# Kernel optimization log

Hardware: AMD Instinct MI355X
Metric: run time of the kernel (lower is better)

## Reference

```python
import jax, jax.numpy as jnp
import numpy as np

DIM = 1024
NUM_HEADS = 16
HEAD_DIM = DIM // NUM_HEADS  # 64
NB_FEATURES = 256


def setup_inputs() -> dict:
    key = jax.random.key(0)
    k1, k2, k3, k4, k5 = jax.random.split(key, 5)
    x = jax.random.normal(k1, (4, 4096, DIM), dtype=jnp.float32)
    # Dense(dim*3, use_bias=False): weight [dim, 3*dim]
    w_qkv = jax.random.normal(k2, (DIM, 3 * DIM), dtype=jnp.float32) / np.sqrt(DIM)
    # Dense(dim) with bias: weight [dim, dim], bias [dim]
    w_out = jax.random.normal(k3, (DIM, DIM), dtype=jnp.float32) / np.sqrt(DIM)
    b_out = jnp.zeros((DIM,), dtype=jnp.float32)
    # random_normal_initializer default stddev=0.05
    proj = 0.05 * jax.random.normal(k4, (NUM_HEADS, HEAD_DIM, NB_FEATURES), dtype=jnp.float32)
    return {"x": x, "w_qkv": w_qkv, "w_out": w_out, "b_out": b_out, "proj": proj}


def _kernel_feature_map(x, proj):
    # x: [B,H,T,D], proj: [H,D,F] -> [B,H,T,F]
    z = jnp.einsum('bhtd,hdf->bhtf', x, proj)
    return jnp.exp(z - jnp.max(z, axis=-1, keepdims=True))


def reference(x, w_qkv, w_out, b_out, proj):
    B, T, _ = x.shape
    qkv = x @ w_qkv  # [B,T,3*DIM]
    q, k, v = jnp.split(qkv, 3, axis=-1)
    # [B,T,H,D] -> [B,H,T,D]
    def to_heads(t):
        return t.reshape(B, T, NUM_HEADS, HEAD_DIM).transpose(0, 2, 1, 3)
    q, k, v = to_heads(q), to_heads(k), to_heads(v)
    q_prime = _kernel_feature_map(q, proj)  # [B,H,T,F]
    k_prime = _kernel_feature_map(k, proj)  # [B,H,T,F]
    kv = jnp.einsum('bhtf,bhtd->bhfd', k_prime, v)  # [B,H,F,D]
    k_sum = jnp.sum(k_prime, axis=2)  # [B,H,F]
    z = 1.0 / (jnp.einsum('bhtf,bhf->bht', q_prime, k_sum) + 1e-6)
    out = jnp.einsum('bhtf,bhfd,bht->bhtd', q_prime, kv, z)
    out = out.transpose(0, 2, 1, 3).reshape(B, T, DIM)
    return out @ w_out + b_out
```

## Files before the change

### kernel.cpp

```cpp
#include <hip/hip_runtime.h>

#define TOK   16384
#define DIM_  1024
#define QKV_N 3072
#define NH    16
#define HD    64
#define NF    256
#define TSEQ  4096
#define NCHUNK 8
#define CH_T  512
#define KVS   68

typedef __attribute__((ext_vector_type(8))) short  bfrag8;
typedef __attribute__((ext_vector_type(4))) float  ffrag4;
typedef __attribute__((ext_vector_type(8))) unsigned short u16x8;
typedef __attribute__((ext_vector_type(4))) unsigned short u16x4;

__device__ __forceinline__ float bf2f(unsigned short u) {
  union { unsigned int i; float f; } c; c.i = ((unsigned int)u) << 16; return c.f;
}
__device__ __forceinline__ unsigned short f2bf(float f) {
  union { float f; unsigned int i; } c; c.f = f;
  unsigned int r = c.i + 0x7FFFu + ((c.i >> 16) & 1u);
  return (unsigned short)(r >> 16);
}

__device__ __forceinline__ void gload16(const unsigned short* g, unsigned short* l) {
  __builtin_amdgcn_global_load_lds(
      (const __attribute__((address_space(1))) unsigned int*)g,
      (__attribute__((address_space(3))) unsigned int*)l, 16, 0, 0);
}

__global__ __launch_bounds__(256)
void transpose_cast(const float* __restrict__ in, unsigned short* __restrict__ out,
                    int R, int C) {
  __shared__ float tile[32][33];
  const size_t batch_off = (size_t)blockIdx.z * R * C;
  const float* bin = in + batch_off;
  unsigned short* bout = out + batch_off;
  const int bc = blockIdx.x * 32, br = blockIdx.y * 32;
  const int tx = threadIdx.x & 31, ty = threadIdx.x >> 5;
  #pragma unroll
  for (int i = 0; i < 32; i += 8)
    tile[ty + i][tx] = bin[(size_t)(br + ty + i) * C + bc + tx];
  __syncthreads();
  #pragma unroll
  for (int i = 0; i < 32; i += 8)
    bout[(size_t)(bc + ty + i) * R + br + tx] = f2bf(tile[tx][ty + i]);
}

__global__ __launch_bounds__(256)
void split_cast(const float* __restrict__ x, unsigned short* __restrict__ a2) {
  const size_t idx = ((size_t)blockIdx.x * 256 + threadIdx.x) * 8;
  const size_t r = idx >> 10;
  const int c = (int)(idx & 1023);
  const float4 v0 = *(const float4*)&x[idx];
  const float4 v1 = *(const float4*)&x[idx + 4];
  const float f[8] = {v0.x, v0.y, v0.z, v0.w, v1.x, v1.y, v1.z, v1.w};
  u16x8 hi, lo;
  #pragma unroll
  for (int e = 0; e < 8; e++) {
    union { float f; unsigned u; } cc; cc.f = f[e];
    const unsigned short h = (unsigned short)(cc.u >> 16);
    union { unsigned u; float f; } hb; hb.u = ((unsigned)h) << 16;
    hi[e] = h; lo[e] = f2bf(f[e] - hb.f);
  }
  *(u16x8*)&a2[r * 2048 + c] = hi;
  *(u16x8*)&a2[r * 2048 + 1024 + c] = lo;
}

#define GPHASE(Q, STG, VMW)                                                        \
  {                                                                                \
    const int ab = arow + (Q) * 2048;                                              \
    bfrag8 a00 = *(const bfrag8*)&lds[b][0][ab + cA0];                             \
    bfrag8 a01 = *(const bfrag8*)&lds[b][0][ab + cA1];                             \
    bfrag8 a10 = *(const bfrag8*)&lds[b][0][ab + 1024 + cA0];                      \
    bfrag8 a11 = *(const bfrag8*)&lds[b][0][ab + 1024 + cA1];                      \
    if ((Q) == 0) {                                                                \
      _Pragma("unroll")                                                            \
      for (int j = 0; j < 4; j++) {                                                \
        bfr[j][0] = *(const bfrag8*)&lds[b][1][brow + j * 1024 + cA0];             \
        bfr[j][1] = *(const bfrag8*)&lds[b][1][brow + j * 1024 + cA1];             \
      }                                                                            \
    }                                                                              \
    STG;                                                                           \
    __builtin_amdgcn_s_barrier();                                                  \
    __builtin_amdgcn_s_setprio(1);                                                 \
    _Pragma("unroll")                                                              \
    for (int j = 0; j < 4; j++) {                                                  \
      acc[(Q)*2][j]   = __builtin_amdgcn_mfma_f32_16x16x32_bf16(a00, bfr[j][0], acc[(Q)*2][j], 0, 0, 0);   \
      acc[(Q)*2][j]   = __builtin_amdgcn_mfma_f32_16x16x32_bf16(a01, bfr[j][1], acc[(Q)*2][j], 0, 0, 0);   \
      acc[(Q)*2+1][j] = __builtin_amdgcn_mfma_f32_16x16x32_bf16(a10, bfr[j][0], acc[(Q)*2+1][j], 0, 0, 0); \
      acc[(Q)*2+1][j] = __builtin_amdgcn_mfma_f32_16x16x32_bf16(a11, bfr[j][1], acc[(Q)*2+1][j], 0, 0, 0); \
    }                                                                              \
    __builtin_amdgcn_s_setprio(0);                                                 \
    asm volatile("s_waitcnt lgkmcnt(0)" ::: "memory");                             \
    VMW;                                                                           \
    __builtin_amdgcn_s_barrier();                                                  \
  }

template<bool BIAS, typename OutT>
__global__ __launch_bounds__(512, 2)
void gemm256(const unsigned short* __restrict__ A,
             const unsigned short* __restrict__ BT,
             const float* __restrict__ bias, OutT* __restrict__ C,
             int M, int N, int K, int KB) {
  __shared__ alignas(16) unsigned short lds[2][2][256 * 64];
  const int tid = threadIdx.x;
  const int w = tid >> 6, lane = tid & 63;
  const int wm = w >> 2, wn = w & 3;
  const int lq = lane >> 4, lr = lane & 15;

  const int nbx = N >> 8;
  const int cpx = (int)gridDim.x >> 3;
  const int bid = (int)blockIdx.x;
  const int swz = (bid & 7) * cpx + (bid >> 3);
  const int m0 = (swz / nbx) << 8;
  const int n0 = (swz % nbx) << 8;
  const int nkt = K >> 6;
  const int mskB = (KB >> 6) - 1;

  const int sr = tid >> 3;
  const int sc = ((tid & 7) ^ (sr & 7)) << 3;
  const unsigned short* gA = A + (size_t)(m0 + sr) * K + sc;
  const unsigned short* gB = BT + (size_t)(n0 + sr) * KB + sc;

  const int swl = (lr & 7) << 3;
  const int cA0 = (lq * 8) ^ swl;
  const int cA1 = (32 + lq * 8) ^ swl;
  const int arow = (wm * 128 + lr) * 64;
  const int brow = (wn * 64 + lr) * 64;

  ffrag4 acc[8][4] = {};
  bfrag8 bfr[4][2];

  auto stage = [&](int bb, int mat, int h, int kt) {
    const int kk = mat ? (kt & mskB) : kt;
    const int str = mat ? KB : K;
    const unsigned short* g = (mat ? gB : gA) + (size_t)(h * 128) * str + (size_t)kk * 64;
    unsigned short* l = &lds[bb][mat][h * 8192 + tid * 8];
    gload16(g, l);
    gload16(g + (size_t)64 * str, l + 4096);
  };

  stage(0, 0, 0, 0); stage(0, 0, 1, 0);
  stage(0, 1, 0, 0); stage(0, 1, 1, 0);
  stage(1, 1, 0, 1); stage(1, 1, 1, 1);
  asm volatile("s_waitcnt vmcnt(4)" ::: "memory");
  __builtin_amdgcn_s_barrier();

  for (int t = 0; t < nkt; ++t) {
    const int b = t & 1;
    const int bn = b ^ 1;
    GPHASE(0, { if (t + 1 < nkt) stage(bn, 0, 0, t + 1); }, {})
    GPHASE(1, { if (t + 1 < nkt) stage(bn, 0, 1, t + 1); }, {})
    GPHASE(2, { if (t + 2 < nkt) stage(b, 1, 0, t + 2); }, {})
    GPHASE(3, { if (t + 2 < nkt) stage(b, 1, 1, t + 2); },
           { if (t < nkt - 2) { asm volatile("s_waitcnt vmcnt(4)" ::: "memory"); }
             else             { asm volatile("s_waitcnt vmcnt(0)" ::: "memory"); } })
  }

  #pragma unroll
  for (int i = 0; i < 8; i++) {
    const int row = m0 + wm * 128 + i * 16 + lq * 4;
    #pragma unroll
    for (int j = 0; j < 4; j++) {
      const int col = n0 + wn * 64 + j * 16 + lr;
      const float bb = BIAS ? bias[col] : 0.f;
      #pragma unroll
      for (int r = 0; r < 4; r++) {
        const float val = acc[i][j][r] + bb;
        if constexpr (sizeof(OutT) == 2) C[(size_t)(row + r) * N + col] = (OutT)f2bf(val);
        else                             C[(size_t)(row + r) * N + col] = (OutT)val;
      }
    }
  }
}

__global__ __launch_bounds__(256, 2)
void kv_mfma_kernel(const unsigned short* __restrict__ qkv,
                    const unsigned short* __restrict__ projT,
                    float* __restrict__ partial) {
  const int c = blockIdx.x, bh = blockIdx.y;
  const int b = bh >> 4, h = bh & 15;
  const int tid = threadIdx.x;
  const int w = tid >> 6, lane = tid & 63;
  const int lq = lane >> 4, lr = lane & 15;
  __shared__ unsigned short kp[256 * 72];
  __shared__ unsigned short vT[80 * 72];
  __shared__ float wmax[64][4];

  const unsigned short* pTg = projT + (size_t)h * (NF * HD);
  bfrag8 bfgP[2][4];
  #pragma unroll
  for (int kc = 0; kc < 2; kc++)
    #pragma unroll
    for (int j = 0; j < 4; j++)
      bfgP[kc][j] = *(const bfrag8*)&pTg[(size_t)(w * 64 + j * 16 + lr) * 64 + kc * 32 + lq * 8];

  for (int idx = tid; idx < 16 * 72; idx += 256) {
    const int r = idx / 72, cc = idx % 72;
    vT[(64 + r) * 72 + cc] = (r == 0 && cc < 64) ? (unsigned short)0x3F80 : (unsigned short)0;
  }
  __syncthreads();

  ffrag4 acc2[4][5];
  #pragma unroll
  for (int i = 0; i < 4; i++)
    #pragma unroll
    for (int j = 0; j < 5; j++) acc2[i][j] = (ffrag4){0.f, 0.f, 0.f, 0.f};

  const size_t rowbase = (size_t)b * TSEQ + (size_t)c * CH_T;

  for (int tt = 0; tt < CH_T / 64; tt++) {
    const int t0 = tt * 64;
    #pragma unroll
    for (int e = 0; e < 2; e++) {
      const int job = e * 256 + tid;
      const int t = job >> 3, d0 = (job & 7) * 8;
      const u16x8 v = *(const u16x8*)&qkv[(rowbase + t0 + t) * QKV_N + 2048 + h * 64 + d0];
      #pragma unroll
      for (int q = 0; q < 8; q++) vT[(d0 + q) * 72 + t] = v[q];
    }
    ffrag4 accZ[4][4];
    #pragma unroll
    for (int i = 0; i < 4; i++)
      #pragma unroll
      for (int j = 0; j < 4; j++) accZ[i][j] = (ffrag4){0.f, 0.f, 0.f, 0.f};
    #pragma unroll
    for (int kc = 0; kc < 2; kc++) {
      bfrag8 af[4];
      #pragma unroll
      for (int i = 0; i < 4; i++)
        af[i] = *(const bfrag8*)&qkv[(rowbase + t0 + i * 16 + lr) * QKV_N + 1024 + h * 64 + kc * 32 + lq * 8];
      #pragma unroll
      for (int i = 0; i < 4; i++)
        #pragma unroll
        for (int j = 0; j < 4; j++)
          accZ[i][j] = __builtin_amdgcn_mfma_f32_16x16x32_bf16(af[i], bfgP[kc][j], accZ[i][j], 0, 0, 0);
    }
    float pmx[4][4];
    #pragma unroll
    for (int i = 0; i < 4; i++)
      #pragma unroll
      for (int r = 0; r < 4; r++) {
        float m = accZ[i][0][r];
        m = fmaxf(m, accZ[i][1][r]); m = fmaxf(m, accZ[i][2][r]); m = fmaxf(m, accZ[i][3][r]);
        pmx[i][r] = m;
      }
    #pragma unroll
    for (int off = 1; off < 16; off <<= 1)
      #pragma unroll
      for (int i = 0; i < 4; i++)
        #pragma unroll
        for (int r = 0; r < 4; r++)
          pmx[i][r] = fmaxf(pmx[i][r], __shfl_xor(pmx[i][r], off, 64));
    if (lr == 0)
      #pragma unroll
      for (int i = 0; i < 4; i++)
        #pragma unroll
        for (int r = 0; r < 4; r++) wmax[i * 16 + lq * 4 + r][w] = pmx[i][r];
    __syncthreads();
    #pragma unroll
    for (int i = 0; i < 4; i++) {
      float rmarr[4];
      #pragma unroll
      for (int r = 0; r < 4; r++) {
        const float4 wv = *(const float4*)&wmax[i * 16 + lq * 4 + r];
        rmarr[r] = fmaxf(fmaxf(wv.x, wv.y), fmaxf(wv.z, wv.w));
      }
      #pragma unroll
      for (int j = 0; j < 4; j++) {
        u16x4 pk;
        #pragma unroll
        for (int r = 0; r < 4; r++) pk[r] = f2bf(__expf(accZ[i][j][r] - rmarr[r]));
        *(u16x4*)&kp[(w * 64 + j * 16 + lr) * 72 + i * 16 + lq * 4] = pk;
      }
    }
    __syncthreads();
    #pragma unroll
    for (int kc = 0; kc < 2; kc++) {
      bfrag8 af2[4], bf2[5];
      #pragma unroll
      for (int i = 0; i < 4; i++)
        af2[i] = *(const bfrag8*)&kp[(w * 64 + i * 16 + lr) * 72 + kc * 32 + lq * 8];
      #pragma unroll
      for (int j = 0; j < 5; j++)
        bf2[j] = *(const bfrag8*)&vT[(j * 16 + lr) * 72 + kc * 32 + lq * 8];
      #pragma unroll
      for (int i = 0; i < 4; i++)
        #pragma unroll
        for (int j = 0; j < 5; j++)
          acc2[i][j] = __builtin_amdgcn_mfma_f32_16x16x32_bf16(af2[i], bf2[j], acc2[i][j], 0, 0, 0);
    }
    __syncthreads();
  }
  float* pbase = partial + (size_t)(bh * NCHUNK + c) * NF * KVS;
  #pragma unroll
  for (int i = 0; i < 4; i++)
    #pragma unroll
    for (int j = 0; j < 5; j++) {
      if (j == 4 && lr != 0) continue;
      const int col = j * 16 + lr;
      #pragma unroll
      for (int r = 0; r < 4; r++)
        pbase[(size_t)(w * 64 + i * 16 + lq * 4 + r) * KVS + col] = acc2[i][j][r];
    }
}

__global__ __launch_bounds__(256)
void kv_reduce_kernel(const float* __restrict__ partial, float* __restrict__ kv) {
  const size_t i = (size_t)blockIdx.x * 256 + threadIdx.x;
  const size_t per_bh = (size_t)NF * KVS;
  const size_t bh = i / per_bh;
  const size_t j = i % per_bh;
  const float* p = partial + bh * NCHUNK * per_bh + j;
  float s = 0.f;
  #pragma unroll
  for (int c = 0; c < NCHUNK; c++) s += p[c * per_bh];
  kv[i] = s;
}

__global__ __launch_bounds__(256, 2)
void q_attn_mfma_kernel(const unsigned short* __restrict__ qkv,
                        const unsigned short* __restrict__ projT,
                        const float* __restrict__ kv,
                        unsigned short* __restrict__ attn) {
  const int c = blockIdx.x, bh = blockIdx.y;
  const int b = bh >> 4, h = bh & 15;
  const int tid = threadIdx.x;
  const int w = tid >> 6, lane = tid & 63;
  const int lq = lane >> 4, lr = lane & 15;
  __shared__ unsigned short qp[64 * 264];
  __shared__ unsigned short kvT[80 * 264];

  {
    const float* kvrow = kv + ((size_t)bh * NF + tid) * KVS;
    #pragma unroll
    for (int d0 = 0; d0 < 64; d0 += 4) {
      const float4 v = *(const float4*)&kvrow[d0];
      kvT[(d0 + 0) * 264 + tid] = f2bf(v.x);
      kvT[(d0 + 1) * 264 + tid] = f2bf(v.y);
      kvT[(d0 + 2) * 264 + tid] = f2bf(v.z);
      kvT[(d0 + 3) * 264 + tid] = f2bf(v.w);
    }
    kvT[64 * 264 + tid] = f2bf(kvrow[64]);
    for (int idx = tid; idx < 15 * 264; idx += 256)
      kvT[65 * 264 + idx] = 0;
  }
  const unsigned short* pTg = projT + (size_t)h * (NF * HD);
  bfrag8 bfg[2][4];
  #pragma unroll
  for (int kc = 0; kc < 2; kc++)
    #pragma unroll
    for (int j = 0; j < 4; j++)
      bfg[kc][j] = *(const bfrag8*)&pTg[(size_t)(w * 64 + j * 16 + lr) * 64 + kc * 32 + lq * 8];
  __syncthreads();

  for (int tt = 0; tt < CH_T / 64; tt++) {
    const size_t rowbase = (size_t)b * TSEQ + (size_t)c * CH_T + (size_t)tt * 64;
    ffrag4 accZ[4][4];
    #pragma unroll
    for (int i = 0; i < 4; i++)
      #pragma unroll
      for (int j = 0; j < 4; j++) accZ[i][j] = (ffrag4){0.f, 0.f, 0.f, 0.f};
    #pragma unroll
    for (int kc = 0; kc < 2; kc++) {
      bfrag8 af[4];
      #pragma unroll
      for (int i = 0; i < 4; i++)
        af[i] = *(const bfrag8*)&qkv[(rowbase + i * 16 + lr) * QKV_N + 0 + h * 64 + kc * 32 + lq * 8];
      #pragma unroll
      for (int i = 0; i < 4; i++)
        #pragma unroll
        for (int j = 0; j < 4; j++)
          accZ[i][j] = __builtin_amdgcn_mfma_f32_16x16x32_bf16(af[i], bfg[kc][j], accZ[i][j], 0, 0, 0);
    }
    #pragma unroll
    for (int i = 0; i < 4; i++)
      #pragma unroll
      for (int j = 0; j < 4; j++)
        #pragma unroll
        for (int r = 0; r < 4; r++)
          qp[(i * 16 + lq * 4 + r) * 264 + w * 64 + j * 16 + lr] = f2bf(__expf(accZ[i][j][r]));
    __syncthreads();
    ffrag4 acc3[5];
    #pragma unroll
    for (int j = 0; j < 5; j++) acc3[j] = (ffrag4){0.f, 0.f, 0.f, 0.f};
    #pragma unroll
    for (int kc = 0; kc < 8; kc++) {
      const bfrag8 afq = *(const bfrag8*)&qp[(w * 16 + lr) * 264 + kc * 32 + lq * 8];
      #pragma unroll
      for (int j = 0; j < 5; j++) {
        const bfrag8 bf3 = *(const bfrag8*)&kvT[(j * 16 + lr) * 264 + kc * 32 + lq * 8];
        acc3[j] = __builtin_amdgcn_mfma_f32_16x16x32_bf16(afq, bf3, acc3[j], 0, 0, 0);
      }
    }
    #pragma unroll
    for (int r = 0; r < 4; r++) {
      const float den = __shfl(acc3[4][r], lane & 48, 64);
      const float z = 1.f / (den + 1e-6f);
      const int t = c * CH_T + tt * 64 + w * 16 + lq * 4 + r;
      unsigned short* orow = attn + ((size_t)b * TSEQ + t) * DIM_ + h * 64;
      #pragma unroll
      for (int j = 0; j < 4; j++)
        orow[j * 16 + lr] = f2bf(acc3[j][r] * z);
    }
    __syncthreads();
  }
}

extern "C" void kernel_launch(void* const* d_in, const int* in_sizes, int n_in,
                              void* d_out, int out_size, void* d_ws, size_t ws_size,
                              hipStream_t stream) {
  const float* x     = (const float*)d_in[0];
  const float* w_qkv = (const float*)d_in[1];
  const float* w_out = (const float*)d_in[2];
  const float* b_out = (const float*)d_in[3];
  const float* proj  = (const float*)d_in[4];
  float* out = (float*)d_out;

  char* ws = (char*)d_ws;
  unsigned short* qkv    = (unsigned short*)ws;
  float*          partial= (float*)(ws + 100663296);
  unsigned short* attn   = (unsigned short*)(ws + 100663296);
  unsigned short* woutT  = (unsigned short*)(ws + 134217728);
  float*          kvbuf  = (float*)(ws + 136314880);

  const bool full = ws_size >= 174587904ULL;
  unsigned short* a2    = (unsigned short*)(ws + 100663296);
  unsigned short* wqkvT = (unsigned short*)(ws + (full ? 167772160 : 134217728));
  unsigned short* projT = (unsigned short*)(ws + (full ? 174063616 : 140771328));

  transpose_cast<<<dim3(QKV_N/32, DIM_/32, 1), 256, 0, stream>>>(w_qkv, wqkvT, DIM_, QKV_N);
  transpose_cast<<<dim3(NF/32, HD/32, NH), 256, 0, stream>>>(proj, projT, HD, NF);

  if (full) {
    split_cast<<<8192, 256, 0, stream>>>(x, a2);
    gemm256<false, unsigned short><<<768, 512, 0, stream>>>(
        a2, wqkvT, nullptr, qkv, TOK, QKV_N, 2048, 1024);
  } else {
    for (int hh = 0; hh < 2; ++hh) {
      split_cast<<<4096, 256, 0, stream>>>(x + (size_t)hh * 8192 * DIM_, a2);
      gemm256<false, unsigned short><<<384, 512, 0, stream>>>(
          a2, wqkvT, nullptr, qkv + (size_t)hh * 8192 * QKV_N, 8192, QKV_N, 2048, 1024);
    }
  }
  kv_mfma_kernel<<<dim3(NCHUNK, 64), 256, 0, stream>>>(qkv, projT, partial);
  kv_reduce_kernel<<<dim3(64*NF*KVS/256), 256, 0, stream>>>(partial, kvbuf);
  transpose_cast<<<dim3(DIM_/32, DIM_/32, 1), 256, 0, stream>>>(w_out, woutT, DIM_, DIM_);
  q_attn_mfma_kernel<<<dim3(NCHUNK, 64), 256, 0, stream>>>(qkv, projT, kvbuf, attn);
  gemm256<true, float><<<256, 512, 0, stream>>>(attn, woutT, b_out, out, TOK, DIM_, DIM_, DIM_);
}
```

Baseline: 470.2 us.

## Prefetch next V/Q subtile into registers and swizzle vT stores

```diff
diff --git a/kernel.cpp b/kernel.cpp
--- a/kernel.cpp
+++ b/kernel.cpp
@@ -211,16 +211,25 @@
     for (int j = 0; j < 5; j++) acc2[i][j] = (ffrag4){0.f, 0.f, 0.f, 0.f};
 
   const size_t rowbase = (size_t)b * TSEQ + (size_t)c * CH_T;
-
-  for (int tt = 0; tt < CH_T / 64; tt++) {
+  const int vd0 = (tid & 7) * 8;
+  const int vsg = tid & 7;
+  const int vt0 = tid >> 3;
+
+  auto loadV = [&](int tt, u16x8 (&vr)[2]) {
+    #pragma unroll
+    for (int e = 0; e < 2; e++) {
+      const int t = e * 32 + vt0;
+      vr[e] = *(const u16x8*)&qkv[(rowbase + tt * 64 + t) * QKV_N + 2048 + h * 64 + vd0];
+    }
+  };
+
+  auto subtile = [&](int tt, u16x8 (&vcur)[2], u16x8 (&vnxt)[2], bool pf) {
     const int t0 = tt * 64;
     #pragma unroll
     for (int e = 0; e < 2; e++) {
-      const int job = e * 256 + tid;
-      const int t = job >> 3, d0 = (job & 7) * 8;
-      const u16x8 v = *(const u16x8*)&qkv[(rowbase + t0 + t) * QKV_N + 2048 + h * 64 + d0];
-      #pragma unroll
-      for (int q = 0; q < 8; q++) vT[(d0 + q) * 72 + t] = v[q];
+      const int scol = ((e * 32 + vt0) + 8 * vsg) & 63;
+      #pragma unroll
+      for (int q = 0; q < 8; q++) vT[(vd0 + q) * 72 + scol] = vcur[e][q];
     }
     ffrag4 accZ[4][4];
     #pragma unroll
@@ -277,6 +286,7 @@
         *(u16x4*)&kp[(w * 64 + j * 16 + lr) * 72 + i * 16 + lq * 4] = pk;
       }
     }
+    if (pf) loadV(tt + 1, vnxt);
     __syncthreads();
     #pragma unroll
     for (int kc = 0; kc < 2; kc++) {
@@ -285,8 +295,11 @@
       for (int i = 0; i < 4; i++)
         af2[i] = *(const bfrag8*)&kp[(w * 64 + i * 16 + lr) * 72 + kc * 32 + lq * 8];
       #pragma unroll
-      for (int j = 0; j < 5; j++)
-        bf2[j] = *(const bfrag8*)&vT[(j * 16 + lr) * 72 + kc * 32 + lq * 8];
+      for (int j = 0; j < 5; j++) {
+        const int vrow = j * 16 + lr;
+        const int vcol = ((kc * 32 + lq * 8) + 8 * ((2 * j + (lr >> 3)) & 7)) & 63;
+        bf2[j] = *(const bfrag8*)&vT[vrow * 72 + vcol];
+      }
       #pragma unroll
       for (int i = 0; i < 4; i++)
         #pragma unroll
@@ -294,7 +307,15 @@
           acc2[i][j] = __builtin_amdgcn_mfma_f32_16x16x32_bf16(af2[i], bf2[j], acc2[i][j], 0, 0, 0);
     }
     __syncthreads();
-  }
+  };
+
+  u16x8 vA[2], vB[2];
+  loadV(0, vA);
+  for (int uu = 0; uu < CH_T / 64; uu += 2) {
+    subtile(uu,     vA, vB, true);
+    subtile(uu + 1, vB, vA, uu + 2 < CH_T / 64);
+  }
+
   float* pbase = partial + (size_t)(bh * NCHUNK + c) * NF * KVS;
   #pragma unroll
   for (int i = 0; i < 4; i++)
@@ -357,25 +378,28 @@
       bfg[kc][j] = *(const bfrag8*)&pTg[(size_t)(w * 64 + j * 16 + lr) * 64 + kc * 32 + lq * 8];
   __syncthreads();
 
-  for (int tt = 0; tt < CH_T / 64; tt++) {
-    const size_t rowbase = (size_t)b * TSEQ + (size_t)c * CH_T + (size_t)tt * 64;
+  auto loadQ = [&](int tt, bfrag8 (&af)[2][4]) {
+    const size_t rowb = (size_t)b * TSEQ + (size_t)c * CH_T + (size_t)tt * 64;
+    #pragma unroll
+    for (int kc = 0; kc < 2; kc++)
+      #pragma unroll
+      for (int i = 0; i < 4; i++)
+        af[kc][i] = *(const bfrag8*)&qkv[(rowb + i * 16 + lr) * QKV_N + 0 + h * 64 + kc * 32 + lq * 8];
+  };
+
+  auto subtile = [&](int tt, bfrag8 (&cur)[2][4], bfrag8 (&nxt)[2][4], bool pf) {
     ffrag4 accZ[4][4];
     #pragma unroll
     for (int i = 0; i < 4; i++)
       #pragma unroll
       for (int j = 0; j < 4; j++) accZ[i][j] = (ffrag4){0.f, 0.f, 0.f, 0.f};
     #pragma unroll
-    for (int kc = 0; kc < 2; kc++) {
-      bfrag8 af[4];
-      #pragma unroll
-      for (int i = 0; i < 4; i++)
-        af[i] = *(const bfrag8*)&qkv[(rowbase + i * 16 + lr) * QKV_N + 0 + h * 64 + kc * 32 + lq * 8];
+    for (int kc = 0; kc < 2; kc++)
       #pragma unroll
       for (int i = 0; i < 4; i++)
         #pragma unroll
         for (int j = 0; j < 4; j++)
-          accZ[i][j] = __builtin_amdgcn_mfma_f32_16x16x32_bf16(af[i], bfg[kc][j], accZ[i][j], 0, 0, 0);
-    }
+          accZ[i][j] = __builtin_amdgcn_mfma_f32_16x16x32_bf16(cur[kc][i], bfg[kc][j], accZ[i][j], 0, 0, 0);
     #pragma unroll
     for (int i = 0; i < 4; i++)
       #pragma unroll
@@ -383,6 +407,7 @@
         #pragma unroll
         for (int r = 0; r < 4; r++)
           qp[(i * 16 + lq * 4 + r) * 264 + w * 64 + j * 16 + lr] = f2bf(__expf(accZ[i][j][r]));
+    if (pf) loadQ(tt + 1, nxt);
     __syncthreads();
     ffrag4 acc3[5];
     #pragma unroll
@@ -407,6 +432,13 @@
         orow[j * 16 + lr] = f2bf(acc3[j][r] * z);
     }
     __syncthreads();
+  };
+
+  bfrag8 qA[2][4], qB[2][4];
+  loadQ(0, qA);
+  for (int uu = 0; uu < CH_T / 64; uu += 2) {
+    subtile(uu,     qA, qB, true);
+    subtile(uu + 1, qB, qA, uu + 2 < CH_T / 64);
   }
 }
 
```

After: 462.6 us. About the same (-1.6%).
